# Optimization experiments

Hardware: AMD Instinct MI355X
Metric: run time of the kernel (lower is better)

## Reference

```python
import jax, jax.numpy as jnp
import numpy as np

DIM = 1024
HEADS = 16
DIM_HEAD = 64
INNER = HEADS * DIM_HEAD  # 1024
SCALE = DIM_HEAD ** -0.5


def setup_inputs() -> dict:
    key = jax.random.key(0)
    ks = jax.random.split(key, 6)
    b, n = 4, 2048
    x = jax.random.normal(ks[0], (b, n, DIM), dtype=jnp.float32)
    gamma = jnp.ones((DIM,), dtype=jnp.float32)
    # weights stored (in, out); torch Linear computes x @ W.T with W (out, in)
    w_q = jax.random.normal(ks[1], (DIM, INNER), dtype=jnp.float32) * (DIM ** -0.5)
    w_kv = jax.random.normal(ks[2], (DIM, 2 * INNER), dtype=jnp.float32) * (DIM ** -0.5)
    w_out = jax.random.normal(ks[3], (INNER, DIM), dtype=jnp.float32) * (INNER ** -0.5)
    null_kv = jax.random.normal(ks[4], (2, HEADS, 1, DIM_HEAD), dtype=jnp.float32)
    return {"x": x, "gamma": gamma, "w_q": w_q, "w_kv": w_kv, "w_out": w_out, "null_kv": null_kv}


def _layer_norm(x, gamma):
    mu = jnp.mean(x, axis=-1, keepdims=True)
    var = jnp.var(x, axis=-1, keepdims=True)
    return (x - mu) * jax.lax.rsqrt(var + 1e-5) * gamma  # beta == 0


def reference(x, gamma, w_q, w_kv, w_out, null_kv):
    b, n, _ = x.shape
    xn = _layer_norm(x, gamma)
    q = xn @ w_q  # [b, n, inner]
    kv = xn @ w_kv
    k, v = jnp.split(kv, 2, axis=-1)
    q = q * SCALE

    def to_heads(t):
        return t.reshape(b, n, HEADS, DIM_HEAD).transpose(0, 2, 1, 3)  # b h n d

    q, k, v = map(to_heads, (q, k, v))
    nk = jnp.broadcast_to(null_kv[0][None], (b, HEADS, 1, DIM_HEAD))
    nv = jnp.broadcast_to(null_kv[1][None], (b, HEADS, 1, DIM_HEAD))
    k = jnp.concatenate([nk, k], axis=2)  # b h (n+1) d
    v = jnp.concatenate([nv, v], axis=2)
    sim = jnp.einsum('bhid,bhjd->bhij', q, k)
    attn = jax.nn.softmax(sim, axis=-1)
    out = jnp.einsum('bhij,bhjd->bhid', attn, v)
    out = out.transpose(0, 2, 1, 3).reshape(b, n, INNER)
    return out @ w_out
```

## Files before the change

### kernel.cpp

```cpp
#include <hip/hip_runtime.h>

typedef unsigned short ushort_t;
using f32x4  = __attribute__((ext_vector_type(4))) float;
using bf16x8 = __attribute__((ext_vector_type(8))) __bf16;

typedef __attribute__((address_space(1))) const void gvoid_t;
typedef __attribute__((address_space(3))) void svoid_t;

union Frag {
    uint4    u4;
    bf16x8   b;
    ushort_t s[8];
};

__device__ __forceinline__ ushort_t f2bf(float f) {
    union { float f; unsigned u; } a; a.f = f;
    unsigned u = a.u;
    unsigned r = (u + 0x7fffu + ((u >> 16) & 1u)) >> 16;
    return (ushort_t)r;
}
__device__ __forceinline__ float bf2f(ushort_t b) {
    union { unsigned u; float f; } a; a.u = ((unsigned)b) << 16;
    return a.f;
}
__device__ __forceinline__ unsigned pack2bf(float lo, float hi) {
    union { __bf16 h[2]; unsigned u; } p;
    p.h[0] = (__bf16)lo;
    p.h[1] = (__bf16)hi;
    return p.u;
}

__global__ __launch_bounds__(256)
void ln_kernel(const float* __restrict__ x, const float* __restrict__ gamma,
               ushort_t* __restrict__ xn)
{
    const int row = blockIdx.x;
    const int tid = threadIdx.x;
    const float4 v = *reinterpret_cast<const float4*>(x + (size_t)row * 1024 + tid * 4);

    float s = v.x + v.y + v.z + v.w;
    float q = v.x * v.x + v.y * v.y + v.z * v.z + v.w * v.w;
    #pragma unroll
    for (int off = 1; off <= 32; off <<= 1) {
        s += __shfl_xor(s, off);
        q += __shfl_xor(q, off);
    }
    __shared__ float ss[4], sq[4];
    if ((tid & 63) == 0) { ss[tid >> 6] = s; sq[tid >> 6] = q; }
    __syncthreads();
    const float S  = ss[0] + ss[1] + ss[2] + ss[3];
    const float Q  = sq[0] + sq[1] + sq[2] + sq[3];
    const float mu = S * (1.0f / 1024.0f);
    const float var = Q * (1.0f / 1024.0f) - mu * mu;
    const float rstd = rsqrtf(var + 1e-5f);

    const float4 gm = *reinterpret_cast<const float4*>(gamma + tid * 4);
    ushort4 o;
    o.x = f2bf((v.x - mu) * rstd * gm.x);
    o.y = f2bf((v.y - mu) * rstd * gm.y);
    o.z = f2bf((v.z - mu) * rstd * gm.z);
    o.w = f2bf((v.w - mu) * rstd * gm.w);
    *reinterpret_cast<ushort4*>(xn + (size_t)row * 1024 + tid * 4) = o;
}

__global__ __launch_bounds__(256)
void wt_kernel(const float* __restrict__ w, ushort_t* __restrict__ wt, int K, int N)
{
    __shared__ float tile[32][33];
    const int n0 = blockIdx.x * 32, k0 = blockIdx.y * 32;
    const int tx = threadIdx.x, ty = threadIdx.y;
    #pragma unroll
    for (int i = 0; i < 4; ++i) {
        int r = ty + i * 8;
        tile[r][tx] = w[(size_t)(k0 + r) * N + n0 + tx];
    }
    __syncthreads();
    #pragma unroll
    for (int i = 0; i < 4; ++i) {
        int r = ty + i * 8;
        wt[(size_t)(n0 + r) * K + k0 + tx] = f2bf(tile[tx][r]);
    }
}

template<int MODE>
__global__ __launch_bounds__(256)
void gemm_kernel(const ushort_t* __restrict__ A, const ushort_t* __restrict__ Bt,
                 ushort_t* __restrict__ o16a, ushort_t* __restrict__ o16b,
                 float* __restrict__ o32)
{
    __shared__ ushort_t ldsA[128 * 64];
    __shared__ ushort_t ldsB[128 * 64];

    const int tid = threadIdx.x;
    const int n0 = blockIdx.x * 128, m0 = blockIdx.y * 128;
    const int w = tid >> 6, l = tid & 63, g = l >> 4, c = l & 15;
    const int wm = w >> 1, wn = w & 1;

    const ushort_t* asrc[4];
    const ushort_t* bsrc[4];
    #pragma unroll
    for (int j = 0; j < 4; ++j) {
        const int gidx = j * 256 + tid;
        const int row = gidx >> 3;
        const int sl  = (gidx & 7) ^ (row & 7);
        asrc[j] = A  + (size_t)(m0 + row) * 1024 + sl * 8;
        bsrc[j] = Bt + (size_t)(n0 + row) * 1024 + sl * 8;
    }

    f32x4 acc[4][4];
    #pragma unroll
    for (int mi = 0; mi < 4; ++mi)
        #pragma unroll
        for (int ni = 0; ni < 4; ++ni)
            acc[mi][ni] = (f32x4){0.f, 0.f, 0.f, 0.f};

    const int swz = c & 7;

    for (int kt = 0; kt < 16; ++kt) {
        if (kt) __syncthreads();
        #pragma unroll
        for (int j = 0; j < 4; ++j) {
            __builtin_amdgcn_global_load_lds((gvoid_t*)(asrc[j] + kt * 64),
                                             (svoid_t*)(&ldsA[(j * 256 + tid) * 8]), 16, 0, 0);
            __builtin_amdgcn_global_load_lds((gvoid_t*)(bsrc[j] + kt * 64),
                                             (svoid_t*)(&ldsB[(j * 256 + tid) * 8]), 16, 0, 0);
        }
        __syncthreads();

        #pragma unroll
        for (int kk = 0; kk < 2; ++kk) {
            Frag af[4], bfr[4];
            #pragma unroll
            for (int mi = 0; mi < 4; ++mi)
                af[mi].u4 = *reinterpret_cast<const uint4*>(
                    &ldsA[(wm * 64 + mi * 16 + c) * 64 + ((((kk << 2) | g)) ^ swz) * 8]);
            #pragma unroll
            for (int ni = 0; ni < 4; ++ni)
                bfr[ni].u4 = *reinterpret_cast<const uint4*>(
                    &ldsB[(wn * 64 + ni * 16 + c) * 64 + ((((kk << 2) | g)) ^ swz) * 8]);
            #pragma unroll
            for (int mi = 0; mi < 4; ++mi)
                #pragma unroll
                for (int ni = 0; ni < 4; ++ni)
                    acc[mi][ni] = __builtin_amdgcn_mfma_f32_16x16x32_bf16(
                        af[mi].b, bfr[ni].b, acc[mi][ni], 0, 0, 0);
        }
    }

    #pragma unroll
    for (int mi = 0; mi < 4; ++mi) {
        const int mbase = m0 + wm * 64 + mi * 16 + g * 4;
        #pragma unroll
        for (int ni = 0; ni < 4; ++ni) {
            const int n = n0 + wn * 64 + ni * 16 + c;
            if (MODE == 0) {
                const int hh = n >> 6, d = n & 63;
                #pragma unroll
                for (int r = 0; r < 4; ++r) {
                    const int m = mbase + r;
                    const int b = m >> 11, tok = m & 2047;
                    o16a[(((size_t)b * 16 + hh) * 2048 + tok) * 64 + d] =
                        f2bf(acc[mi][ni][r] * 0.125f);
                }
            } else if (MODE == 1) {
                if (n < 1024) {
                    const int hh = n >> 6, d = n & 63;
                    #pragma unroll
                    for (int r = 0; r < 4; ++r) {
                        const int m = mbase + r;
                        const int b = m >> 11, tok = m & 2047;
                        o16a[(((size_t)b * 16 + hh) * 2048 + tok) * 64 + d] =
                            f2bf(acc[mi][ni][r]);
                    }
                } else {
                    const int nn = n - 1024;
                    const int hh = nn >> 6, d = nn & 63;
                    const int b = mbase >> 11, tok0 = mbase & 2047;
                    ushort4 pv;
                    pv.x = f2bf(acc[mi][ni][0]);
                    pv.y = f2bf(acc[mi][ni][1]);
                    pv.z = f2bf(acc[mi][ni][2]);
                    pv.w = f2bf(acc[mi][ni][3]);
                    *reinterpret_cast<ushort4*>(
                        o16b + (((size_t)b * 16 + hh) * 64 + d) * 2048 + tok0) = pv;
                }
            } else {
                #pragma unroll
                for (int r = 0; r < 4; ++r)
                    o32[(size_t)(mbase + r) * 1024 + n] = acc[mi][ni][r];
            }
        }
    }
}

__global__ __launch_bounds__(512)
void attn_kernel(const ushort_t* __restrict__ q, const ushort_t* __restrict__ k,
                 const ushort_t* __restrict__ vt, const float* __restrict__ nkv,
                 ushort_t* __restrict__ out)
{
    __shared__ ushort_t kvs[2][8192];
    __shared__ unsigned plds[8][16 * 32];

    const int tid = threadIdx.x;
    const int w = tid >> 6, l = tid & 63, g = l >> 4, c = l & 15;
    const int qb = blockIdx.x, bh = blockIdx.y, h = bh & 15;

    const ushort_t* kb = k  + (size_t)bh * 2048 * 64;
    const ushort_t* vb = vt + (size_t)bh * 64 * 2048;

    const int srow = tid >> 3;
    const int ssl  = (tid & 7) ^ (srow & 7);
    const ushort_t* ksrc = kb + srow * 64 + ssl * 8;
    const ushort_t* vsrc = vb + srow * 2048 + ssl * 8;

    const ushort_t* qbase = q + ((size_t)bh * 2048 + qb * 128 + w * 16) * 64;
    Frag aq[2];
    #pragma unroll
    for (int kk = 0; kk < 2; ++kk)
        aq[kk].u4 = *reinterpret_cast<const uint4*>(qbase + c * 64 + kk * 32 + g * 8);

    float snull = 0.f;
    #pragma unroll
    for (int kk = 0; kk < 2; ++kk) {
        const float4 n0 = *reinterpret_cast<const float4*>(nkv + h * 64 + kk * 32 + g * 8);
        const float4 n1 = *reinterpret_cast<const float4*>(nkv + h * 64 + kk * 32 + g * 8 + 4);
        snull += bf2f(aq[kk].s[0]) * n0.x + bf2f(aq[kk].s[1]) * n0.y
               + bf2f(aq[kk].s[2]) * n0.z + bf2f(aq[kk].s[3]) * n0.w;
        snull += bf2f(aq[kk].s[4]) * n1.x + bf2f(aq[kk].s[5]) * n1.y
               + bf2f(aq[kk].s[6]) * n1.z + bf2f(aq[kk].s[7]) * n1.w;
    }
    snull += __shfl_xor(snull, 16);
    snull += __shfl_xor(snull, 32);

    float m_run  = snull;
    float l_part = (l < 16) ? 1.f : 0.f;

    f32x4 acc[4];
    #pragma unroll
    for (int nf = 0; nf < 4; ++nf) {
        const float nv = nkv[1024 + h * 64 + nf * 16 + c];
        #pragma unroll
        for (int r = 0; r < 4; ++r) acc[nf][r] = nv;
    }

    unsigned* pw = &plds[w][0] + c * 32;
    const int swz  = c & 7;
    const int swzP = (c & 7) << 2;

    __builtin_amdgcn_global_load_lds((gvoid_t*)(ksrc), (svoid_t*)(&kvs[0][tid * 8]), 16, 0, 0);
    __builtin_amdgcn_global_load_lds((gvoid_t*)(vsrc), (svoid_t*)(&kvs[0][4096 + tid * 8]), 16, 0, 0);
    __syncthreads();

    int cur = 0;
    for (int t = 0; t < 32; ++t) {
        if (t < 31) {
            __builtin_amdgcn_global_load_lds((gvoid_t*)(ksrc + (t + 1) * 4096),
                                             (svoid_t*)(&kvs[cur ^ 1][tid * 8]), 16, 0, 0);
            __builtin_amdgcn_global_load_lds((gvoid_t*)(vsrc + (t + 1) * 64),
                                             (svoid_t*)(&kvs[cur ^ 1][4096 + tid * 8]), 16, 0, 0);
        }
        const ushort_t* kbuf = &kvs[cur][0];
        const ushort_t* vbuf = &kvs[cur][4096];

        Frag bk[4][2];
        #pragma unroll
        for (int nt = 0; nt < 4; ++nt)
            #pragma unroll
            for (int kk = 0; kk < 2; ++kk)
                bk[nt][kk].u4 = *reinterpret_cast<const uint4*>(
                    &kbuf[(nt * 16 + c) * 64 + (((kk << 2) | g) ^ swz) * 8]);

        f32x4 st[4];
        __builtin_amdgcn_s_setprio(1);
        #pragma unroll
        for (int nt = 0; nt < 4; ++nt) {
            f32x4 z = (f32x4){0.f, 0.f, 0.f, 0.f};
            st[nt] = __builtin_amdgcn_mfma_f32_16x16x32_bf16(bk[nt][0].b, aq[0].b, z, 0, 0, 0);
            st[nt] = __builtin_amdgcn_mfma_f32_16x16x32_bf16(bk[nt][1].b, aq[1].b, st[nt], 0, 0, 0);
        }
        __builtin_amdgcn_s_setprio(0);

        Frag bv[4][2];
        #pragma unroll
        for (int nf = 0; nf < 4; ++nf)
            #pragma unroll
            for (int k2 = 0; k2 < 2; ++k2)
                bv[nf][k2].u4 = *reinterpret_cast<const uint4*>(
                    &vbuf[(nf * 16 + c) * 64 + (((k2 << 2) | g) ^ swz) * 8]);

        float m01 = fmaxf(fmaxf(st[0][0], st[0][1]), fmaxf(st[0][2], st[0][3]));
        float m23 = fmaxf(fmaxf(st[1][0], st[1][1]), fmaxf(st[1][2], st[1][3]));
        float m45 = fmaxf(fmaxf(st[2][0], st[2][1]), fmaxf(st[2][2], st[2][3]));
        float m67 = fmaxf(fmaxf(st[3][0], st[3][1]), fmaxf(st[3][2], st[3][3]));
        float pm = fmaxf(fmaxf(m01, m23), fmaxf(m45, m67));
        pm = fmaxf(pm, __shfl_xor(pm, 16));
        pm = fmaxf(pm, __shfl_xor(pm, 32));

        if (__any(pm > m_run + 8.f)) {
            const float nm = fmaxf(m_run, pm);
            const float alpha = __expf(m_run - nm);
            m_run = nm;
            l_part *= alpha;
            float av[4];
            #pragma unroll
            for (int r = 0; r < 4; ++r) av[r] = __shfl(alpha, g * 4 + r);
            #pragma unroll
            for (int nf = 0; nf < 4; ++nf)
                #pragma unroll
                for (int r = 0; r < 4; ++r)
                    acc[nf][r] *= av[r];
        }

        #pragma unroll
        for (int nt = 0; nt < 4; ++nt)
            #pragma unroll
            for (int r = 0; r < 4; ++r)
                st[nt][r] = __expf(st[nt][r] - m_run);

        float s0 = (st[0][0] + st[0][1]) + (st[0][2] + st[0][3]);
        float s1 = (st[1][0] + st[1][1]) + (st[1][2] + st[1][3]);
        float s2 = (st[2][0] + st[2][1]) + (st[2][2] + st[2][3]);
        float s3 = (st[3][0] + st[3][1]) + (st[3][2] + st[3][3]);
        l_part += (s0 + s1) + (s2 + s3);

        #pragma unroll
        for (int nt = 0; nt < 4; ++nt) {
            uint2 pr;
            pr.x = pack2bf(st[nt][0], st[nt][1]);
            pr.y = pack2bf(st[nt][2], st[nt][3]);
            *reinterpret_cast<uint2*>(&pw[(nt * 8 + 2 * g) ^ swzP]) = pr;
        }

        Frag pa[2];
        #pragma unroll
        for (int k2 = 0; k2 < 2; ++k2)
            pa[k2].u4 = *reinterpret_cast<const uint4*>(&pw[(k2 * 16 + 4 * g) ^ swzP]);

        __builtin_amdgcn_s_setprio(1);
        #pragma unroll
        for (int nf = 0; nf < 4; ++nf) {
            acc[nf] = __builtin_amdgcn_mfma_f32_16x16x32_bf16(pa[0].b, bv[nf][0].b, acc[nf], 0, 0, 0);
            acc[nf] = __builtin_amdgcn_mfma_f32_16x16x32_bf16(pa[1].b, bv[nf][1].b, acc[nf], 0, 0, 0);
        }
        __builtin_amdgcn_s_setprio(0);

        __syncthreads();
        cur ^= 1;
    }

    l_part += __shfl_xor(l_part, 16);
    l_part += __shfl_xor(l_part, 32);

    const size_t ob = ((size_t)(bh >> 4) * 2048 + qb * 128 + w * 16) * 1024 + h * 64;
    #pragma unroll
    for (int r = 0; r < 4; ++r) {
        const float inv = 1.f / __shfl(l_part, g * 4 + r);
        #pragma unroll
        for (int nf = 0; nf < 4; ++nf)
            out[ob + (size_t)(g * 4 + r) * 1024 + nf * 16 + c] = f2bf(acc[nf][r] * inv);
    }
}

extern "C" void kernel_launch(void* const* d_in, const int* in_sizes, int n_in,
                              void* d_out, int out_size, void* d_ws, size_t ws_size,
                              hipStream_t stream)
{
    (void)in_sizes; (void)n_in; (void)out_size; (void)ws_size;
    const float* x     = (const float*)d_in[0];
    const float* gamma = (const float*)d_in[1];
    const float* w_q   = (const float*)d_in[2];
    const float* w_kv  = (const float*)d_in[3];
    const float* w_out = (const float*)d_in[4];
    const float* nkv   = (const float*)d_in[5];
    float* out = (float*)d_out;

    char* ws = (char*)d_ws;
    ushort_t* xn   = (ushort_t*)(ws);
    ushort_t* wqT  = (ushort_t*)(ws + 16777216);
    ushort_t* wkvT = (ushort_t*)(ws + 18874368);
    ushort_t* woT  = (ushort_t*)(ws + 23068672);
    ushort_t* qh   = (ushort_t*)(ws + 25165824);
    ushort_t* kh   = (ushort_t*)(ws + 41943040);
    ushort_t* vtb  = (ushort_t*)(ws + 58720256);
    ushort_t* ao   = xn;

    ln_kernel<<<dim3(8192), dim3(256), 0, stream>>>(x, gamma, xn);
    wt_kernel<<<dim3(32, 32), dim3(32, 8), 0, stream>>>(w_q,  wqT, 1024, 1024);
    wt_kernel<<<dim3(64, 32), dim3(32, 8), 0, stream>>>(w_kv, wkvT, 1024, 2048);
    wt_kernel<<<dim3(32, 32), dim3(32, 8), 0, stream>>>(w_out, woT, 1024, 1024);

    gemm_kernel<0><<<dim3(8, 64),  dim3(256), 0, stream>>>(xn, wqT,  qh, nullptr, nullptr);
    gemm_kernel<1><<<dim3(16, 64), dim3(256), 0, stream>>>(xn, wkvT, kh, vtb, nullptr);

    attn_kernel<<<dim3(16, 64), dim3(512), 0, stream>>>(qh, kh, vtb, nkv, ao);

    gemm_kernel<2><<<dim3(8, 64), dim3(256), 0, stream>>>(ao, woT, nullptr, nullptr, out);
}
```

Baseline: 245.9 us.

## Keep attention P in registers via transposed MFMA, use exp2 and reorder grids

The attention kernel now computes the transposed output so that the bf16 softmax probabilities feed a 16x16x16 MFMA straight from registers. This removes the per-tile LDS write and read of P, and the K/V fragments are loaded just before use instead of all up front. The Q scale folds in log2(e) so the kernel can use the hardware exp2, and the rescale threshold is raised to 12, which leaves larger unnormalised exponents in the accumulators. Grid axes are swapped for the GEMMs and attention, changing block scheduling order and cache reuse. The output store is vectorised, and launch bounds request higher occupancy.

```diff
diff --git a/kernel.cpp b/kernel.cpp
--- a/kernel.cpp
+++ b/kernel.cpp
@@ -1,8 +1,11 @@
 #include <hip/hip_runtime.h>
 
 typedef unsigned short ushort_t;
-using f32x4  = __attribute__((ext_vector_type(4))) float;
-using bf16x8 = __attribute__((ext_vector_type(8))) __bf16;
+using f32x4   = __attribute__((ext_vector_type(4))) float;
+using bf16x8  = __attribute__((ext_vector_type(8))) __bf16;
+using bf16x4  = __attribute__((ext_vector_type(4))) __bf16;
+using short4_t = __attribute__((ext_vector_type(4))) short;
+using u32x2   = __attribute__((ext_vector_type(2))) unsigned;
 
 typedef __attribute__((address_space(1))) const void gvoid_t;
 typedef __attribute__((address_space(3))) void svoid_t;
@@ -12,6 +15,12 @@
     bf16x8   b;
     ushort_t s[8];
 };
+union Frag2 {
+    u32x2    u2;
+    bf16x4   b;
+    short4_t s4;
+    unsigned u[2];
+};
 
 __device__ __forceinline__ ushort_t f2bf(float f) {
     union { float f; unsigned u; } a; a.f = f;
@@ -29,6 +38,27 @@
     p.h[1] = (__bf16)hi;
     return p.u;
 }
+__device__ __forceinline__ float exp2_fast(float x) {
+#if __has_builtin(__builtin_amdgcn_exp2f)
+    return __builtin_amdgcn_exp2f(x);
+#else
+    return exp2f(x);
+#endif
+}
+__device__ __forceinline__ f32x4 mfma16(Frag2 a, Frag2 b, f32x4 c) {
+#if __has_builtin(__builtin_amdgcn_mfma_f32_16x16x16_bf16)
+    return __builtin_amdgcn_mfma_f32_16x16x16_bf16(a.b, b.b, c, 0, 0, 0);
+#elif __has_builtin(__builtin_amdgcn_mfma_f32_16x16x16bf16_1k)
+    return __builtin_amdgcn_mfma_f32_16x16x16bf16_1k(a.s4, b.s4, c, 0, 0, 0);
+#else
+    f32x4 d;
+    asm("v_mfma_f32_16x16x16_bf16 %0, %1, %2, %3"
+        : "=v"(d) : "v"(a.u2), "v"(b.u2), "v"(c));
+    return d;
+#endif
+}
+
+#define QSCALE 0.18033688011112042f
 
 __global__ __launch_bounds__(256)
 void ln_kernel(const float* __restrict__ x, const float* __restrict__ gamma,
@@ -92,7 +122,7 @@
     __shared__ ushort_t ldsB[128 * 64];
 
     const int tid = threadIdx.x;
-    const int n0 = blockIdx.x * 128, m0 = blockIdx.y * 128;
+    const int m0 = blockIdx.x * 128, n0 = blockIdx.y * 128;
     const int w = tid >> 6, l = tid & 63, g = l >> 4, c = l & 15;
     const int wm = w >> 1, wn = w & 1;
 
@@ -160,7 +190,7 @@
                     const int m = mbase + r;
                     const int b = m >> 11, tok = m & 2047;
                     o16a[(((size_t)b * 16 + hh) * 2048 + tok) * 64 + d] =
-                        f2bf(acc[mi][ni][r] * 0.125f);
+                        f2bf(acc[mi][ni][r] * QSCALE);
                 }
             } else if (MODE == 1) {
                 if (n < 1024) {
@@ -193,17 +223,16 @@
     }
 }
 
-__global__ __launch_bounds__(512)
+__global__ __launch_bounds__(512, 8)
 void attn_kernel(const ushort_t* __restrict__ q, const ushort_t* __restrict__ k,
                  const ushort_t* __restrict__ vt, const float* __restrict__ nkv,
                  ushort_t* __restrict__ out)
 {
     __shared__ ushort_t kvs[2][8192];
-    __shared__ unsigned plds[8][16 * 32];
 
     const int tid = threadIdx.x;
     const int w = tid >> 6, l = tid & 63, g = l >> 4, c = l & 15;
-    const int qb = blockIdx.x, bh = blockIdx.y, h = bh & 15;
+    const int bh = blockIdx.x, qb = blockIdx.y, h = bh & 15;
 
     const ushort_t* kb = k  + (size_t)bh * 2048 * 64;
     const ushort_t* vb = vt + (size_t)bh * 64 * 2048;
@@ -238,14 +267,11 @@
     f32x4 acc[4];
     #pragma unroll
     for (int nf = 0; nf < 4; ++nf) {
-        const float nv = nkv[1024 + h * 64 + nf * 16 + c];
-        #pragma unroll
-        for (int r = 0; r < 4; ++r) acc[nf][r] = nv;
-    }
-
-    unsigned* pw = &plds[w][0] + c * 32;
-    const int swz  = c & 7;
-    const int swzP = (c & 7) << 2;
+        const float4 nv = *reinterpret_cast<const float4*>(nkv + 1024 + h * 64 + nf * 16 + g * 4);
+        acc[nf] = (f32x4){nv.x, nv.y, nv.z, nv.w};
+    }
+
+    const int swz = c & 7;
 
     __builtin_amdgcn_global_load_lds((gvoid_t*)(ksrc), (svoid_t*)(&kvs[0][tid * 8]), 16, 0, 0);
     __builtin_amdgcn_global_load_lds((gvoid_t*)(vsrc), (svoid_t*)(&kvs[0][4096 + tid * 8]), 16, 0, 0);
@@ -262,31 +288,20 @@
         const ushort_t* kbuf = &kvs[cur][0];
         const ushort_t* vbuf = &kvs[cur][4096];
 
-        Frag bk[4][2];
-        #pragma unroll
-        for (int nt = 0; nt < 4; ++nt)
-            #pragma unroll
-            for (int kk = 0; kk < 2; ++kk)
-                bk[nt][kk].u4 = *reinterpret_cast<const uint4*>(
-                    &kbuf[(nt * 16 + c) * 64 + (((kk << 2) | g) ^ swz) * 8]);
-
         f32x4 st[4];
         __builtin_amdgcn_s_setprio(1);
         #pragma unroll
         for (int nt = 0; nt < 4; ++nt) {
+            Frag bk0, bk1;
+            bk0.u4 = *reinterpret_cast<const uint4*>(
+                &kbuf[(nt * 16 + c) * 64 + ((g) ^ swz) * 8]);
+            bk1.u4 = *reinterpret_cast<const uint4*>(
+                &kbuf[(nt * 16 + c) * 64 + ((4 | g) ^ swz) * 8]);
             f32x4 z = (f32x4){0.f, 0.f, 0.f, 0.f};
-            st[nt] = __builtin_amdgcn_mfma_f32_16x16x32_bf16(bk[nt][0].b, aq[0].b, z, 0, 0, 0);
-            st[nt] = __builtin_amdgcn_mfma_f32_16x16x32_bf16(bk[nt][1].b, aq[1].b, st[nt], 0, 0, 0);
+            st[nt] = __builtin_amdgcn_mfma_f32_16x16x32_bf16(bk0.b, aq[0].b, z, 0, 0, 0);
+            st[nt] = __builtin_amdgcn_mfma_f32_16x16x32_bf16(bk1.b, aq[1].b, st[nt], 0, 0, 0);
         }
         __builtin_amdgcn_s_setprio(0);
-
-        Frag bv[4][2];
-        #pragma unroll
-        for (int nf = 0; nf < 4; ++nf)
-            #pragma unroll
-            for (int k2 = 0; k2 < 2; ++k2)
-                bv[nf][k2].u4 = *reinterpret_cast<const uint4*>(
-                    &vbuf[(nf * 16 + c) * 64 + (((k2 << 2) | g) ^ swz) * 8]);
 
         float m01 = fmaxf(fmaxf(st[0][0], st[0][1]), fmaxf(st[0][2], st[0][3]));
         float m23 = fmaxf(fmaxf(st[1][0], st[1][1]), fmaxf(st[1][2], st[1][3]));
@@ -296,26 +311,23 @@
         pm = fmaxf(pm, __shfl_xor(pm, 16));
         pm = fmaxf(pm, __shfl_xor(pm, 32));
 
-        if (__any(pm > m_run + 8.f)) {
+        if (__any(pm > m_run + 12.f)) {
             const float nm = fmaxf(m_run, pm);
-            const float alpha = __expf(m_run - nm);
+            const float alpha = exp2_fast(m_run - nm);
             m_run = nm;
             l_part *= alpha;
-            float av[4];
-            #pragma unroll
-            for (int r = 0; r < 4; ++r) av[r] = __shfl(alpha, g * 4 + r);
             #pragma unroll
             for (int nf = 0; nf < 4; ++nf)
                 #pragma unroll
                 for (int r = 0; r < 4; ++r)
-                    acc[nf][r] *= av[r];
+                    acc[nf][r] *= alpha;
         }
 
         #pragma unroll
         for (int nt = 0; nt < 4; ++nt)
             #pragma unroll
             for (int r = 0; r < 4; ++r)
-                st[nt][r] = __expf(st[nt][r] - m_run);
+                st[nt][r] = exp2_fast(st[nt][r] - m_run);
 
         float s0 = (st[0][0] + st[0][1]) + (st[0][2] + st[0][3]);
         float s1 = (st[1][0] + st[1][1]) + (st[1][2] + st[1][3]);
@@ -323,24 +335,24 @@
         float s3 = (st[3][0] + st[3][1]) + (st[3][2] + st[3][3]);
         l_part += (s0 + s1) + (s2 + s3);
 
+        Frag2 pb[4];
         #pragma unroll
         for (int nt = 0; nt < 4; ++nt) {
-            uint2 pr;
-            pr.x = pack2bf(st[nt][0], st[nt][1]);
-            pr.y = pack2bf(st[nt][2], st[nt][3]);
-            *reinterpret_cast<uint2*>(&pw[(nt * 8 + 2 * g) ^ swzP]) = pr;
-        }
-
-        Frag pa[2];
-        #pragma unroll
-        for (int k2 = 0; k2 < 2; ++k2)
-            pa[k2].u4 = *reinterpret_cast<const uint4*>(&pw[(k2 * 16 + 4 * g) ^ swzP]);
+            pb[nt].u[0] = pack2bf(st[nt][0], st[nt][1]);
+            pb[nt].u[1] = pack2bf(st[nt][2], st[nt][3]);
+        }
 
         __builtin_amdgcn_s_setprio(1);
         #pragma unroll
         for (int nf = 0; nf < 4; ++nf) {
-            acc[nf] = __builtin_amdgcn_mfma_f32_16x16x32_bf16(pa[0].b, bv[nf][0].b, acc[nf], 0, 0, 0);
-            acc[nf] = __builtin_amdgcn_mfma_f32_16x16x32_bf16(pa[1].b, bv[nf][1].b, acc[nf], 0, 0, 0);
+            const ushort_t* vrow = vbuf + (nf * 16 + c) * 64;
+            #pragma unroll
+            for (int nt = 0; nt < 4; ++nt) {
+                Frag2 va;
+                va.u2 = *reinterpret_cast<const u32x2*>(
+                    &vrow[(((nt << 1) | (g >> 1)) ^ swz) * 8 + (g & 1) * 4]);
+                acc[nf] = mfma16(va, pb[nt], acc[nf]);
+            }
         }
         __builtin_amdgcn_s_setprio(0);
 
@@ -350,14 +362,15 @@
 
     l_part += __shfl_xor(l_part, 16);
     l_part += __shfl_xor(l_part, 32);
-
-    const size_t ob = ((size_t)(bh >> 4) * 2048 + qb * 128 + w * 16) * 1024 + h * 64;
-    #pragma unroll
-    for (int r = 0; r < 4; ++r) {
-        const float inv = 1.f / __shfl(l_part, g * 4 + r);
-        #pragma unroll
-        for (int nf = 0; nf < 4; ++nf)
-            out[ob + (size_t)(g * 4 + r) * 1024 + nf * 16 + c] = f2bf(acc[nf][r] * inv);
+    const float inv = 1.f / l_part;
+
+    ushort_t* ob = out + ((size_t)(bh >> 4) * 2048 + qb * 128 + w * 16 + c) * 1024 + h * 64;
+    #pragma unroll
+    for (int nf = 0; nf < 4; ++nf) {
+        uint2 ov;
+        ov.x = pack2bf(acc[nf][0] * inv, acc[nf][1] * inv);
+        ov.y = pack2bf(acc[nf][2] * inv, acc[nf][3] * inv);
+        *reinterpret_cast<uint2*>(ob + nf * 16 + g * 4) = ov;
     }
 }
 
@@ -389,10 +402,10 @@
     wt_kernel<<<dim3(64, 32), dim3(32, 8), 0, stream>>>(w_kv, wkvT, 1024, 2048);
     wt_kernel<<<dim3(32, 32), dim3(32, 8), 0, stream>>>(w_out, woT, 1024, 1024);
 
-    gemm_kernel<0><<<dim3(8, 64),  dim3(256), 0, stream>>>(xn, wqT,  qh, nullptr, nullptr);
-    gemm_kernel<1><<<dim3(16, 64), dim3(256), 0, stream>>>(xn, wkvT, kh, vtb, nullptr);
-
-    attn_kernel<<<dim3(16, 64), dim3(512), 0, stream>>>(qh, kh, vtb, nkv, ao);
-
-    gemm_kernel<2><<<dim3(8, 64), dim3(256), 0, stream>>>(ao, woT, nullptr, nullptr, out);
-}
+    gemm_kernel<0><<<dim3(64, 8),  dim3(256), 0, stream>>>(xn, wqT,  qh, nullptr, nullptr);
+    gemm_kernel<1><<<dim3(64, 16), dim3(256), 0, stream>>>(xn, wkvT, kh, vtb, nullptr);
+
+    attn_kernel<<<dim3(64, 16), dim3(512), 0, stream>>>(qh, kh, vtb, nkv, ao);
+
+    gemm_kernel<2><<<dim3(64, 8), dim3(256), 0, stream>>>(ao, woT, nullptr, nullptr, out);
+}
```

Result: slower. 256.5 us (+4.3%).
